# Kernel optimization log

Measured on AMD Instinct MI355X. Metric: run time of the kernel, lower is better.

The kernel has to match this reference:

```python
import jax, jax.numpy as jnp
import numpy as np

_SAMPLING_EPS = 1e-05
_FP16_TINY = float(np.finfo(np.float16).tiny)  # masked_fill value used by the torch code


def _token_mask(tokens, num_seqs, vocab_size):
    # bin-count via scatter-add into width vocab+1 (padding id == vocab), then mask
    rows = jnp.arange(num_seqs)[:, None]
    counts = jnp.zeros((num_seqs, vocab_size + 1), jnp.int32).at[rows, tokens].add(1)
    return counts[:, :vocab_size] > 0


def setup_inputs() -> dict:
    key = jax.random.key(0)
    ks = jax.random.split(key, 9)
    B, V, PL, OL = 128, 128000, 2048, 256
    logits = jax.random.normal(ks[0], (B, V), dtype=jnp.float32) * 4.0
    prompt_tokens = jax.random.randint(ks[1], (B, PL), 0, V, dtype=jnp.int64)
    output_tokens = jax.random.randint(ks[2], (B, OL), 0, V, dtype=jnp.int64)
    presence_penalties = jax.random.uniform(ks[3], (B,), dtype=jnp.float32)
    frequency_penalties = jax.random.uniform(ks[4], (B,), dtype=jnp.float32)
    repetition_penalties = 1.0 + 0.3 * jax.random.uniform(ks[5], (B,), dtype=jnp.float32)
    temperature = 0.1 + 0.9 * jax.random.uniform(ks[6], (B,), dtype=jnp.float32)
    top_k = jax.random.randint(ks[7], (B,), 1, 100, dtype=jnp.int64)
    top_p = 0.5 + 0.49 * jax.random.uniform(ks[8], (B,), dtype=jnp.float32)
    return {
        "logits": logits,
        "prompt_tokens": prompt_tokens,
        "output_tokens": output_tokens,
        "presence_penalties": presence_penalties,
        "frequency_penalties": frequency_penalties,
        "repetition_penalties": repetition_penalties,
        "temperature": temperature,
        "top_k": top_k,
        "top_p": top_p,
    }


def reference(logits, prompt_tokens, output_tokens, presence_penalties,
              frequency_penalties, repetition_penalties, temperature,
              top_k, top_p):
    B, V = logits.shape
    logits = logits.astype(jnp.float32)

    # --- penalties (NOTE: torch code computes frequency counts but never applies
    # frequency_penalties; we faithfully do the same) ---
    prompt_mask = _token_mask(prompt_tokens, B, V)
    output_mask = _token_mask(output_tokens, B, V)
    pen = jnp.where(prompt_mask | output_mask, repetition_penalties[:, None], 1.0)
    logits = jnp.where(logits > 0, logits / pen, logits * pen)
    logits = logits - presence_penalties[:, None] * output_mask.astype(jnp.float32)

    # --- temperature ---
    temp = jnp.where(temperature < _SAMPLING_EPS, 1.0, temperature)
    logits = logits / temp[:, None]

    # --- top-k / top-p via ascending sort (mirrors torch implementation) ---
    idx = jnp.argsort(logits, axis=-1)                      # ascending
    ls = jnp.take_along_axis(logits, idx, axis=-1)
    thr_pos = (V - top_k.astype(jnp.int32))[:, None]
    thr = jnp.take_along_axis(ls, thr_pos, axis=-1)         # [B,1]
    ls = jnp.where(ls < thr, _FP16_TINY, ls)
    probs_sort = jax.nn.softmax(ls, axis=-1)
    csum = jnp.cumsum(probs_sort, axis=-1)
    tp_mask = csum <= (1.0 - top_p)[:, None]
    tp_mask = tp_mask.at[:, -1].set(False)
    ls = jnp.where(tp_mask, _FP16_TINY, ls)

    # unsort back to original vocab order
    rows = jnp.arange(B)[:, None]
    out_logits = jnp.zeros_like(logits).at[rows, idx].set(ls)

    probs = jax.nn.softmax(out_logits, axis=-1)
    return probs, prompt_mask, output_mask
```

## Files before the change

### kernel.cpp

```cpp
#include <hip/hip_runtime.h>
#include <math.h>

#define B   128
#define V   128000
#define WPR 4000
#define PL  2048
#define OL  256
#define BPR 25
#define ITERS 5
#define TLOC 128
#define CAP  6144
#define FP16_TINY 6.103515625e-05f

typedef float f4_nt __attribute__((ext_vector_type(4)));
__device__ __forceinline__ void nt_store4(float* p, float a, float b, float c, float d) {
    f4_nt v = {a, b, c, d};
    __builtin_nontemporal_store(v, (f4_nt*)p);
}

__device__ __forceinline__ unsigned key_of(float f) {
    unsigned u = __float_as_uint(f);
    unsigned m = (unsigned)(((int)u) >> 31) | 0x80000000u;
    return u ^ m;
}
__device__ __forceinline__ float key_inv(unsigned k) {
    unsigned u = (k & 0x80000000u) ? (k ^ 0x80000000u) : ~k;
    return __uint_as_float(u);
}

__device__ __forceinline__ float xform(float x, int pm, int om,
                                       float rep, float pres, float temp) {
#pragma clang fp contract(off)
    float pen = (pm | om) ? rep : 1.0f;
    float l = (x > 0.0f) ? (x / pen) : (x * pen);
    if (om) l = l - pres;
    return l / temp;
}

__global__ __launch_bounds__(256) void k_zero(unsigned* __restrict__ p, int n) {
    int i = blockIdx.x * 256 + threadIdx.x;
    int stride = gridDim.x * 256;
    for (; i < n; i += stride) p[i] = 0u;
}

__global__ __launch_bounds__(256) void k_scatter(const int* __restrict__ ptok,
                                                 const int* __restrict__ otok,
                                                 unsigned* __restrict__ bitP,
                                                 unsigned* __restrict__ bitO) {
    int i = blockIdx.x * 256 + threadIdx.x;
    int np = B * PL;
    int total = np + B * OL;
    if (i >= total) return;
    if (i < np) {
        int r = i >> 11;
        int t = ptok[i];
        if ((unsigned)t < (unsigned)V)
            atomicOr(&bitP[r * WPR + (t >> 5)], 1u << (t & 31));
    } else {
        int j = i - np;
        int r = j >> 8;
        int t = otok[j];
        if ((unsigned)t < (unsigned)V)
            atomicOr(&bitO[r * WPR + (t >> 5)], 1u << (t & 31));
    }
}

__global__ __launch_bounds__(256) void k_main(
    const float* __restrict__ logits,
    const unsigned* __restrict__ bitP, const unsigned* __restrict__ bitO,
    const float* __restrict__ rep, const float* __restrict__ pres,
    const float* __restrict__ temp,
    float* __restrict__ outPm, float* __restrict__ outOm,
    unsigned* __restrict__ cnt, unsigned long long* __restrict__ cand)
{
    __shared__ unsigned h[4096];
    __shared__ unsigned sA[256];
    __shared__ int s_beta;
    __shared__ unsigned s_base;
    int r = blockIdx.y;
    int c0 = blockIdx.x * (ITERS * 1024);
    int t = threadIdx.x;
    for (int i = t; i < 4096; i += 256) h[i] = 0u;
    __syncthreads();
    float rp = rep[r], pp = pres[r];
    float tt = temp[r]; tt = (tt < 1e-5f) ? 1.0f : tt;
    const float* lrow = logits + (size_t)r * V;
    float* pmrow = outPm + (size_t)r * V;
    float* omrow = outOm + (size_t)r * V;
    const unsigned* bp = bitP + r * WPR;
    const unsigned* bo = bitO + r * WPR;
    float4 lv[ITERS];
#pragma unroll
    for (int it = 0; it < ITERS; it++) {
        int i = c0 + it * 1024 + t * 4;
        float4 x = *(const float4*)(lrow + i);
        unsigned wp = bp[i >> 5], wo = bo[i >> 5];
        int sh = i & 31;
        float xs[4] = {x.x, x.y, x.z, x.w};
        float res[4], fp[4], fo[4];
#pragma unroll
        for (int j = 0; j < 4; j++) {
            int p = (wp >> (sh + j)) & 1;
            int o = (wo >> (sh + j)) & 1;
            float l = xform(xs[j], p, o, rp, pp, tt);
            atomicAdd(&h[key_of(l) >> 20], 1u);
            res[j] = l; fp[j] = (float)p; fo[j] = (float)o;
        }
        lv[it] = make_float4(res[0], res[1], res[2], res[3]);
        nt_store4(pmrow + i, fp[0], fp[1], fp[2], fp[3]);
        nt_store4(omrow + i, fo[0], fo[1], fo[2], fo[3]);
    }
    __syncthreads();
    unsigned cs = 0;
#pragma unroll
    for (int j = 0; j < 16; j++) cs += h[t * 16 + j];
    sA[t] = cs;
    __syncthreads();
    unsigned v = cs;
    for (int st = 1; st < 256; st <<= 1) {
        unsigned add = (t + st < 256) ? sA[t + st] : 0u;
        __syncthreads();
        v += add; sA[t] = v;
        __syncthreads();
    }
    unsigned Snext = (t < 255) ? sA[t + 1] : 0u;
    if (sA[t] >= TLOC && Snext < TLOC) {
        unsigned run = Snext;
        int beta = t * 16;
        for (int j = 15; j >= 0; j--) {
            run += h[t * 16 + j];
            if (run >= TLOC) { beta = t * 16 + j; break; }
        }
        s_beta = beta;
    }
    __syncthreads();
    unsigned beta = (unsigned)s_beta;
    unsigned myc = 0;
#pragma unroll
    for (int it = 0; it < ITERS; it++) {
        float xs[4] = {lv[it].x, lv[it].y, lv[it].z, lv[it].w};
#pragma unroll
        for (int j = 0; j < 4; j++)
            if ((key_of(xs[j]) >> 20) >= beta) myc++;
    }
    sA[t] = myc;
    __syncthreads();
    unsigned pv = myc;
    for (int st = 1; st < 256; st <<= 1) {
        unsigned add = (t >= st) ? sA[t - st] : 0u;
        __syncthreads();
        pv += add; sA[t] = pv;
        __syncthreads();
    }
    if (t == 255) s_base = atomicAdd(&cnt[r], pv);
    __syncthreads();
    unsigned w = s_base + (pv - myc);
#pragma unroll
    for (int it = 0; it < ITERS; it++) {
        float xs[4] = {lv[it].x, lv[it].y, lv[it].z, lv[it].w};
#pragma unroll
        for (int j = 0; j < 4; j++) {
            unsigned key = key_of(xs[j]);
            if ((key >> 20) >= beta) {
                if (w < (unsigned)CAP) {
                    int idx = c0 + it * 1024 + t * 4 + j;
                    cand[(size_t)r * CAP + w] =
                        ((unsigned long long)key << 32) | (unsigned)idx;
                }
                w++;
            }
        }
    }
}

__global__ __launch_bounds__(256) void k_select(
    const unsigned* __restrict__ cnt, const unsigned long long* __restrict__ cand,
    const int* __restrict__ topk, const float* __restrict__ topp,
    float4* __restrict__ params, int* __restrict__ idxc)
{
    __shared__ unsigned long long list[CAP];
    __shared__ unsigned long long kv[256];
    __shared__ unsigned rh[256];
    __shared__ unsigned rsuf[256];
    __shared__ double sD[256];
    __shared__ unsigned s_prefix, s_krem, s_kcnt;
    int r = blockIdx.x;
    int t = threadIdx.x;
    int n = (int)min(cnt[r], (unsigned)CAP);
    const unsigned long long* crow = cand + (size_t)r * CAP;
    for (int i = t; i < n; i += 256) list[i] = crow[i];
    int k = topk[r]; k = max(1, min(k, 127));
    if (t == 0) { s_prefix = 0u; s_krem = (unsigned)k; }
    __syncthreads();
    for (int round = 3; round >= 0; round--) {
        int shift = round * 8;
        unsigned prefix = s_prefix;
        unsigned krem = s_krem;
        unsigned maskAbove = (round == 3) ? 0u : (0xFFFFFFFFu << (shift + 8));
        rh[t] = 0u;
        __syncthreads();
        for (int i = t; i < n; i += 256) {
            unsigned key = (unsigned)(list[i] >> 32);
            if ((key & maskAbove) == (prefix & maskAbove))
                atomicAdd(&rh[(key >> shift) & 255u], 1u);
        }
        __syncthreads();
        unsigned vv = rh[t];
        rsuf[t] = vv;
        __syncthreads();
        for (int st = 1; st < 256; st <<= 1) {
            unsigned add = (t + st < 256) ? rsuf[t + st] : 0u;
            __syncthreads();
            vv += add; rsuf[t] = vv;
            __syncthreads();
        }
        unsigned Sx = (t < 255) ? rsuf[t + 1] : 0u;
        if (rsuf[t] >= krem && Sx < krem) {
            s_prefix = prefix | ((unsigned)t << shift);
            s_krem = krem - Sx;
        }
        __syncthreads();
    }
    unsigned thrkey = s_prefix;
    if (t == 0) s_kcnt = 0u;
    __syncthreads();
    for (int i = t; i < n; i += 256) {
        if ((unsigned)(list[i] >> 32) >= thrkey) {
            unsigned pos = atomicAdd(&s_kcnt, 1u);
            if (pos < 256u) kv[pos] = list[i];
        }
    }
    __syncthreads();
    int K = (int)min(s_kcnt, 256u);
    if (t >= K) kv[t] = 0ULL;
    __syncthreads();
    for (unsigned k2 = 2; k2 <= 256; k2 <<= 1) {
        for (unsigned j2 = k2 >> 1; j2 > 0; j2 >>= 1) {
            unsigned ixj = (unsigned)t ^ j2;
            if (ixj > (unsigned)t) {
                unsigned long long a = kv[t], b = kv[ixj];
                bool descBlock = (((unsigned)t & k2) == 0u);
                bool doSwap = descBlock ? (a < b) : (a > b);
                if (doSwap) { kv[t] = b; kv[ixj] = a; }
            }
            __syncthreads();
        }
    }
    float Mxf = key_inv((unsigned)(kv[0] >> 32));
    double MxD = (double)Mxf;
    double e_t = (t < K) ? exp((double)key_inv((unsigned)(kv[t] >> 32)) - MxD)
                         : 0.0;
    sD[t] = e_t;
    __syncthreads();
    for (int st = 128; st > 0; st >>= 1) {
        if (t < st) sD[t] += sD[t + st];
        __syncthreads();
    }
    double S = sD[0];
    __syncthreads();
    double e_tinyD = exp((double)FP16_TINY - MxD);
    double Z1 = (double)(V - K) * e_tinyD + S;
    double base = (double)(V - K) * e_tinyD / Z1;
    double thresh = 1.0 - (double)topp[r];
    sD[t] = e_t;
    __syncthreads();
    double sv = e_t;
    for (int st = 1; st < 256; st <<= 1) {
        double add = (t + st < 256) ? sD[t + st] : 0.0;
        __syncthreads();
        sv += add; sD[t] = sv;
        __syncthreads();
    }
    double suf_t = sv;
    unsigned flag = (t >= 1 && t < K && (base + suf_t / Z1) <= thresh) ? 1u : 0u;
    rsuf[t] = flag;
    __syncthreads();
    for (int st = 128; st > 0; st >>= 1) {
        if (t < st) rsuf[t] += rsuf[t + st];
        __syncthreads();
    }
    int cm = (int)rsuf[0];
    int ns = K - cm;
    sD[t] = (t < ns) ? e_t : 0.0;
    __syncthreads();
    for (int st = 128; st > 0; st >>= 1) {
        if (t < st) sD[t] += sD[t + st];
        __syncthreads();
    }
    if (t == 0) {
        double S2 = sD[0];
        unsigned bkey = (unsigned)(kv[ns - 1] >> 32);
        float v_b = key_inv(bkey);
        unsigned idx_cut = (unsigned)(kv[ns - 1] & 0xFFFFFFFFu);
        float tiny_e = expf(FP16_TINY - Mxf);
        double Z2 = (double)(V - ns) * (double)tiny_e + S2;
        float invZ2 = (float)(1.0 / Z2);
        params[r] = make_float4(v_b, Mxf, invZ2, tiny_e * invZ2);
        idxc[r] = (int)idx_cut;
    }
}

__global__ __launch_bounds__(256) void k_final(
    const float* __restrict__ logits,
    const unsigned* __restrict__ bitP, const unsigned* __restrict__ bitO,
    const float* __restrict__ rep, const float* __restrict__ pres,
    const float* __restrict__ temp,
    const float4* __restrict__ params, const int* __restrict__ idxc,
    float* __restrict__ probs)
{
    int r = blockIdx.y;
    int c0 = blockIdx.x * (ITERS * 1024);
    int t = threadIdx.x;
    float rp = rep[r], pp = pres[r];
    float tt = temp[r]; tt = (tt < 1e-5f) ? 1.0f : tt;
    float4 pr = params[r];
    float v_b = pr.x, Mx = pr.y, invZ2 = pr.z, ptiny = pr.w;
    unsigned idx_cut = (unsigned)idxc[r];
    const float* lrow = logits + (size_t)r * V;
    float* orow = probs + (size_t)r * V;
    const unsigned* bp = bitP + r * WPR;
    const unsigned* bo = bitO + r * WPR;
#pragma unroll
    for (int it = 0; it < ITERS; it++) {
        int i = c0 + it * 1024 + t * 4;
        float4 x = *(const float4*)(lrow + i);
        unsigned wp = bp[i >> 5], wo = bo[i >> 5];
        int sh = i & 31;
        float xs[4] = {x.x, x.y, x.z, x.w};
        float res[4];
#pragma unroll
        for (int j = 0; j < 4; j++) {
            int p = (wp >> (sh + j)) & 1;
            int o = (wo >> (sh + j)) & 1;
            float l = xform(xs[j], p, o, rp, pp, tt);
            bool keep = (l > v_b) || (l == v_b && (unsigned)(i + j) >= idx_cut);
            res[j] = keep ? (expf(l - Mx) * invZ2) : ptiny;
        }
        nt_store4(orow + i, res[0], res[1], res[2], res[3]);
    }
}

extern "C" void kernel_launch(void* const* d_in, const int* in_sizes, int n_in,
                              void* d_out, int out_size, void* d_ws, size_t ws_size,
                              hipStream_t stream) {
    const float* logits = (const float*)d_in[0];
    const int* ptok     = (const int*)d_in[1];
    const int* otok     = (const int*)d_in[2];
    const float* pres   = (const float*)d_in[3];
    const float* rep    = (const float*)d_in[5];
    const float* temp   = (const float*)d_in[6];
    const int* topk     = (const int*)d_in[7];
    const float* topp   = (const float*)d_in[8];

    float* out_probs = (float*)d_out;
    float* out_pm = out_probs + (size_t)B * V;
    float* out_om = out_pm + (size_t)B * V;

    unsigned* ws0 = (unsigned*)d_ws;
    float4* params = (float4*)d_ws;
    int* idxc = (int*)(ws0 + 512);
    unsigned* bitP = ws0 + 768;
    unsigned* bitO = bitP + B * WPR;
    unsigned* cnt  = bitO + B * WPR;
    unsigned long long* cand =
        (unsigned long long*)(cnt + B + 64);

    k_zero<<<256, 256, 0, stream>>>(bitP, 2 * B * WPR + B);

    int ntok = B * PL + B * OL;
    k_scatter<<<(ntok + 255) / 256, 256, 0, stream>>>(ptok, otok, bitP, bitO);

    dim3 g(BPR, B);
    k_main<<<g, 256, 0, stream>>>(logits, bitP, bitO, rep, pres, temp,
                                  out_pm, out_om, cnt, cand);
    k_select<<<B, 256, 0, stream>>>(cnt, cand, topk, topp, params, idxc);
    k_final<<<g, 256, 0, stream>>>(logits, bitP, bitO, rep, pres, temp,
                                   params, idxc, out_probs);
}
```

Measured before the change: 317.5 us.

## Build token bitmaps in shared memory, drop zero kernel, use reciprocal multiplies

The global zero kernel and the global-atomic scatter are replaced by one block per row that builds the prompt and output bitmaps in LDS, then writes them out and resets the row counter. This removes one launch and the global atomics. The penalty and temperature divides become multiplies by precomputed reciprocals, which can change rounding against the reference. k_main also keeps the sort keys in registers instead of recomputing them from the floats.

Result: faster. 309.1 us (-2.6%).

```diff
diff --git a/kernel.cpp b/kernel.cpp
--- a/kernel.cpp
+++ b/kernel.cpp
@@ -29,40 +29,40 @@
 }
 
 __device__ __forceinline__ float xform(float x, int pm, int om,
-                                       float rep, float pres, float temp) {
+                                       float rp, float rrp, float pres, float itt) {
 #pragma clang fp contract(off)
-    float pen = (pm | om) ? rep : 1.0f;
-    float l = (x > 0.0f) ? (x / pen) : (x * pen);
+    float m = (pm | om) ? ((x > 0.0f) ? rrp : rp) : 1.0f;
+    float l = x * m;
     if (om) l = l - pres;
-    return l / temp;
-}
-
-__global__ __launch_bounds__(256) void k_zero(unsigned* __restrict__ p, int n) {
-    int i = blockIdx.x * 256 + threadIdx.x;
-    int stride = gridDim.x * 256;
-    for (; i < n; i += stride) p[i] = 0u;
+    return l * itt;
 }
 
 __global__ __launch_bounds__(256) void k_scatter(const int* __restrict__ ptok,
                                                  const int* __restrict__ otok,
                                                  unsigned* __restrict__ bitP,
-                                                 unsigned* __restrict__ bitO) {
-    int i = blockIdx.x * 256 + threadIdx.x;
-    int np = B * PL;
-    int total = np + B * OL;
-    if (i >= total) return;
-    if (i < np) {
-        int r = i >> 11;
-        int t = ptok[i];
-        if ((unsigned)t < (unsigned)V)
-            atomicOr(&bitP[r * WPR + (t >> 5)], 1u << (t & 31));
-    } else {
-        int j = i - np;
-        int r = j >> 8;
-        int t = otok[j];
-        if ((unsigned)t < (unsigned)V)
-            atomicOr(&bitO[r * WPR + (t >> 5)], 1u << (t & 31));
-    }
+                                                 unsigned* __restrict__ bitO,
+                                                 unsigned* __restrict__ cnt) {
+    __shared__ unsigned mp[WPR];
+    __shared__ unsigned mo[WPR];
+    int r = blockIdx.x;
+    int t = threadIdx.x;
+    for (int i = t; i < WPR; i += 256) { mp[i] = 0u; mo[i] = 0u; }
+    if (t == 0) cnt[r] = 0u;
+    __syncthreads();
+    const int* prow = ptok + (size_t)r * PL;
+    const int* orow = otok + (size_t)r * OL;
+    for (int i = t; i < PL; i += 256) {
+        int tok = prow[i];
+        if ((unsigned)tok < (unsigned)V) atomicOr(&mp[tok >> 5], 1u << (tok & 31));
+    }
+    for (int i = t; i < OL; i += 256) {
+        int tok = orow[i];
+        if ((unsigned)tok < (unsigned)V) atomicOr(&mo[tok >> 5], 1u << (tok & 31));
+    }
+    __syncthreads();
+    unsigned* bpo = bitP + (size_t)r * WPR;
+    unsigned* boo = bitO + (size_t)r * WPR;
+    for (int i = t; i < WPR; i += 256) { bpo[i] = mp[i]; boo[i] = mo[i]; }
 }
 
 __global__ __launch_bounds__(256) void k_main(
@@ -84,12 +84,14 @@
     __syncthreads();
     float rp = rep[r], pp = pres[r];
     float tt = temp[r]; tt = (tt < 1e-5f) ? 1.0f : tt;
+    float rrp = 1.0f / rp;
+    float itt = 1.0f / tt;
     const float* lrow = logits + (size_t)r * V;
     float* pmrow = outPm + (size_t)r * V;
     float* omrow = outOm + (size_t)r * V;
-    const unsigned* bp = bitP + r * WPR;
-    const unsigned* bo = bitO + r * WPR;
-    float4 lv[ITERS];
+    const unsigned* bp = bitP + (size_t)r * WPR;
+    const unsigned* bo = bitO + (size_t)r * WPR;
+    uint4 kv4[ITERS];
 #pragma unroll
     for (int it = 0; it < ITERS; it++) {
         int i = c0 + it * 1024 + t * 4;
@@ -97,16 +99,18 @@
         unsigned wp = bp[i >> 5], wo = bo[i >> 5];
         int sh = i & 31;
         float xs[4] = {x.x, x.y, x.z, x.w};
-        float res[4], fp[4], fo[4];
+        unsigned ks[4];
+        float fp[4], fo[4];
 #pragma unroll
         for (int j = 0; j < 4; j++) {
             int p = (wp >> (sh + j)) & 1;
             int o = (wo >> (sh + j)) & 1;
-            float l = xform(xs[j], p, o, rp, pp, tt);
-            atomicAdd(&h[key_of(l) >> 20], 1u);
-            res[j] = l; fp[j] = (float)p; fo[j] = (float)o;
-        }
-        lv[it] = make_float4(res[0], res[1], res[2], res[3]);
+            float l = xform(xs[j], p, o, rp, rrp, pp, itt);
+            unsigned key = key_of(l);
+            atomicAdd(&h[key >> 20], 1u);
+            ks[j] = key; fp[j] = (float)p; fo[j] = (float)o;
+        }
+        kv4[it] = make_uint4(ks[0], ks[1], ks[2], ks[3]);
         nt_store4(pmrow + i, fp[0], fp[1], fp[2], fp[3]);
         nt_store4(omrow + i, fo[0], fo[1], fo[2], fo[3]);
     }
@@ -138,10 +142,10 @@
     unsigned myc = 0;
 #pragma unroll
     for (int it = 0; it < ITERS; it++) {
-        float xs[4] = {lv[it].x, lv[it].y, lv[it].z, lv[it].w};
+        unsigned ks[4] = {kv4[it].x, kv4[it].y, kv4[it].z, kv4[it].w};
 #pragma unroll
         for (int j = 0; j < 4; j++)
-            if ((key_of(xs[j]) >> 20) >= beta) myc++;
+            if ((ks[j] >> 20) >= beta) myc++;
     }
     sA[t] = myc;
     __syncthreads();
@@ -157,10 +161,10 @@
     unsigned w = s_base + (pv - myc);
 #pragma unroll
     for (int it = 0; it < ITERS; it++) {
-        float xs[4] = {lv[it].x, lv[it].y, lv[it].z, lv[it].w};
+        unsigned ks[4] = {kv4[it].x, kv4[it].y, kv4[it].z, kv4[it].w};
 #pragma unroll
         for (int j = 0; j < 4; j++) {
-            unsigned key = key_of(xs[j]);
+            unsigned key = ks[j];
             if ((key >> 20) >= beta) {
                 if (w < (unsigned)CAP) {
                     int idx = c0 + it * 1024 + t * 4 + j;
@@ -313,13 +317,15 @@
     int t = threadIdx.x;
     float rp = rep[r], pp = pres[r];
     float tt = temp[r]; tt = (tt < 1e-5f) ? 1.0f : tt;
+    float rrp = 1.0f / rp;
+    float itt = 1.0f / tt;
     float4 pr = params[r];
     float v_b = pr.x, Mx = pr.y, invZ2 = pr.z, ptiny = pr.w;
     unsigned idx_cut = (unsigned)idxc[r];
     const float* lrow = logits + (size_t)r * V;
     float* orow = probs + (size_t)r * V;
-    const unsigned* bp = bitP + r * WPR;
-    const unsigned* bo = bitO + r * WPR;
+    const unsigned* bp = bitP + (size_t)r * WPR;
+    const unsigned* bo = bitO + (size_t)r * WPR;
 #pragma unroll
     for (int it = 0; it < ITERS; it++) {
         int i = c0 + it * 1024 + t * 4;
@@ -332,7 +338,7 @@
         for (int j = 0; j < 4; j++) {
             int p = (wp >> (sh + j)) & 1;
             int o = (wo >> (sh + j)) & 1;
-            float l = xform(xs[j], p, o, rp, pp, tt);
+            float l = xform(xs[j], p, o, rp, rrp, pp, itt);
             bool keep = (l > v_b) || (l == v_b && (unsigned)(i + j) >= idx_cut);
             res[j] = keep ? (expf(l - Mx) * invZ2) : ptiny;
         }
@@ -365,10 +371,7 @@
     unsigned long long* cand =
         (unsigned long long*)(cnt + B + 64);
 
-    k_zero<<<256, 256, 0, stream>>>(bitP, 2 * B * WPR + B);
-
-    int ntok = B * PL + B * OL;
-    k_scatter<<<(ntok + 255) / 256, 256, 0, stream>>>(ptok, otok, bitP, bitO);
+    k_scatter<<<B, 256, 0, stream>>>(ptok, otok, bitP, bitO, cnt);
 
     dim3 g(BPR, B);
     k_main<<<g, 256, 0, stream>>>(logits, bitP, bitO, rep, pres, temp,
```
